# Performance work log

Measured on AMD Instinct MI355X. Metric: run time of the kernel, lower is better.

The kernel has to match this reference:

```python
import jax, jax.numpy as jnp
import numpy as np

B, NDOC, L, E = 32, 4, 512, 512
SCALE = np.float32(1.0 / np.sqrt(E))
NEG_INF = np.float32(-1e9)


def setup_inputs() -> dict:
    key = jax.random.key(0)
    k1, k2, k3, k4, k5, k6 = jax.random.split(key, 6)
    return {
        "x1": jax.random.normal(k1, (B, L, E), dtype=jnp.float32),
        "x2": jax.random.normal(k2, (B, NDOC, L, E), dtype=jnp.float32),
        "x1_len": jax.random.randint(k3, (B,), 0, L, dtype=jnp.int64),
        "x2_len": jax.random.randint(k4, (B, NDOC), 0, L, dtype=jnp.int64),
        "fusion_w": jax.random.normal(k5, (2 * E, E), dtype=jnp.float32) * 0.02,
        "fusion_b": jnp.zeros((E,), dtype=jnp.float32),
        "out_w": jax.random.normal(k6, (8 * E, 2 * E), dtype=jnp.float32) * 0.02,
        "out_b": jnp.zeros((2 * E,), dtype=jnp.float32),
    }


def reference(x1, x2, x1_len, x2_len, fusion_w, fusion_b, out_w, out_b):
    # Faithful to torch .repeat(1,4,...): concatenate 4 full copies along batch,
    # so attention row i pairs x1[i % B] with x2[i // 4, i % 4].
    x1_rep = jnp.tile(x1, (NDOC, 1, 1))          # [4B, L, E]
    x2_r = x2.reshape(-1, L, E)                  # [4B, L, E]

    x1_len_r = jnp.tile(x1_len, NDOC)            # [4B] (same tiling as x1_rep)
    x2_len_r = x2_len.reshape(-1)                # [4B]
    pos = jnp.arange(L)
    q_mask = pos[None, :] < x1_len_r[:, None]    # [4B, L]
    k_mask = pos[None, :] < x2_len_r[:, None]    # [4B, L]
    mask = q_mask[:, :, None] & k_mask[:, None, :]  # [4B, L, L]

    # scaled-dot-product attention with masked_fill(mask==0, -1e9)
    scores = jnp.einsum('bqe,bke->bqk', x1_rep, x2_r) * SCALE  # [4B, L, L]
    scores = jnp.where(mask, scores, NEG_INF)
    attn = jax.nn.softmax(scores, axis=-1)
    x1_att = jnp.einsum('bqk,bke->bqe', attn, x2_r)            # [4B, L, E]

    cat = jnp.concatenate([x1_rep - x1_att, x1_rep * x1_att], axis=-1)  # [4B, L, 2E]
    fus = jax.nn.relu(cat @ fusion_w + fusion_b)                        # [4B, L, E]

    x1_mean = jnp.mean(fus, axis=1)              # [4B, E]
    x1_max = jnp.max(fus, axis=1)                # [4B, E]
    pooled = jnp.concatenate([x1_mean.reshape(B, -1), x1_max.reshape(B, -1)], axis=-1)  # [B, 8E]
    out = jax.nn.relu(pooled @ out_w + out_b)    # [B, 2E]
    return out, attn
```

## Files before the change

kernel.cpp:

```cpp
#include <hip/hip_runtime.h>
#include <cstddef>

#define BATCH 32
#define NB    128
#define LL    512
#define EE    512
#define SCALE 0.044194173824159216f
#define NEG_INF -1e9f

typedef __attribute__((ext_vector_type(4))) float f32x4;
typedef __attribute__((ext_vector_type(8))) short s16x8;
typedef __attribute__((ext_vector_type(4))) unsigned short u16x4;

__device__ __forceinline__ unsigned short f2b(float f) {
    unsigned u = __float_as_uint(f);
    u += 0x7FFFu + ((u >> 16) & 1u);
    return (unsigned short)(u >> 16);
}
__device__ __forceinline__ float b2f(unsigned short h) {
    return __uint_as_float(((unsigned)h) << 16);
}

__global__ __launch_bounds__(256) void k_cvt_x1(
    const float* __restrict__ x1, unsigned short* __restrict__ x1bf)
{
    const size_t idx = (size_t)blockIdx.x * 256 + threadIdx.x;
    f32x4 v = *(const f32x4*)(x1 + idx * 4);
    u16x4 o = { f2b(v[0]), f2b(v[1]), f2b(v[2]), f2b(v[3]) };
    *(u16x4*)(x1bf + idx * 4) = o;
}

__global__ __launch_bounds__(256) void k_cvt_x2(
    const float* __restrict__ x2,
    unsigned short* __restrict__ x2bf, unsigned short* __restrict__ x2t)
{
    __shared__ float T[64][65];
    const int i = blockIdx.z, kb = blockIdx.y * 64, eb = blockIdx.x * 64;
    const float* src = x2 + (size_t)i * LL * EE;
    unsigned short* db = x2bf + (size_t)i * LL * EE;
    unsigned short* dt = x2t  + (size_t)i * LL * EE;
    const int t = threadIdx.x, r16 = t >> 4, c4 = (t & 15) * 4;
#pragma unroll
    for (int p = 0; p < 4; ++p) {
        int row = p * 16 + r16;
        f32x4 v = *(const f32x4*)(src + (size_t)(kb + row) * EE + eb + c4);
        T[row][c4] = v[0]; T[row][c4+1] = v[1]; T[row][c4+2] = v[2]; T[row][c4+3] = v[3];
        u16x4 o = { f2b(v[0]), f2b(v[1]), f2b(v[2]), f2b(v[3]) };
        *(u16x4*)(db + (size_t)(kb + row) * EE + eb + c4) = o;
    }
    __syncthreads();
#pragma unroll
    for (int p = 0; p < 4; ++p) {
        int erow = p * 16 + r16;
        u16x4 o = { f2b(T[c4][erow]), f2b(T[c4+1][erow]),
                    f2b(T[c4+2][erow]), f2b(T[c4+3][erow]) };
        *(u16x4*)(dt + (size_t)(eb + erow) * LL + kb + c4) = o;
    }
}

__global__ __launch_bounds__(256) void k_cvt_fw(
    const float* __restrict__ fw, unsigned short* __restrict__ fwt)
{
    __shared__ float T[64][65];
    const int jb = blockIdx.y * 64, eb = blockIdx.x * 64;
    const int t = threadIdx.x, r16 = t >> 4, c4 = (t & 15) * 4;
#pragma unroll
    for (int p = 0; p < 4; ++p) {
        int row = p * 16 + r16;
        f32x4 v = *(const f32x4*)(fw + (size_t)(jb + row) * EE + eb + c4);
        T[row][c4] = v[0]; T[row][c4+1] = v[1]; T[row][c4+2] = v[2]; T[row][c4+3] = v[3];
    }
    __syncthreads();
#pragma unroll
    for (int p = 0; p < 4; ++p) {
        int erow = p * 16 + r16;
        u16x4 o = { f2b(T[c4][erow]), f2b(T[c4+1][erow]),
                    f2b(T[c4+2][erow]), f2b(T[c4+3][erow]) };
        *(u16x4*)(fwt + (size_t)(eb + erow) * 1024 + jb + c4) = o;
    }
}

__global__ __launch_bounds__(256) void k_scores_mfma(
    const unsigned short* __restrict__ x1bf,
    const unsigned short* __restrict__ x2bf,
    const int* __restrict__ x1_len, const int* __restrict__ x2_len,
    float* __restrict__ attn)
{
    __shared__ unsigned short Al[128 * 40];
    __shared__ unsigned short Bl[128 * 40];
    const int i  = blockIdx.z;
    const int q0 = blockIdx.y * 128;
    const int k0 = blockIdx.x * 128;
    const unsigned short* Ag = x1bf + (size_t)(i & 31) * LL * EE;
    const unsigned short* Bg = x2bf + (size_t)i * LL * EE;
    const int t = threadIdx.x, lane = t & 63;
    const int w = t >> 6, wrow = w >> 1, wcol = w & 1;
    const int m = lane & 15, quad = lane >> 4;
    const int srow = t >> 1, shalf = (t & 1) * 16;

    f32x4 acc[4][4];
#pragma unroll
    for (int r = 0; r < 4; ++r)
#pragma unroll
        for (int c = 0; c < 4; ++c) acc[r][c] = (f32x4){0.f, 0.f, 0.f, 0.f};

    for (int e0 = 0; e0 < EE; e0 += 32) {
        s16x8 a0 = *(const s16x8*)(Ag + (size_t)(q0 + srow) * EE + e0 + shalf);
        s16x8 a1 = *(const s16x8*)(Ag + (size_t)(q0 + srow) * EE + e0 + shalf + 8);
        s16x8 b0 = *(const s16x8*)(Bg + (size_t)(k0 + srow) * EE + e0 + shalf);
        s16x8 b1 = *(const s16x8*)(Bg + (size_t)(k0 + srow) * EE + e0 + shalf + 8);
        __syncthreads();
        *(s16x8*)&Al[srow * 40 + shalf]     = a0;
        *(s16x8*)&Al[srow * 40 + shalf + 8] = a1;
        *(s16x8*)&Bl[srow * 40 + shalf]     = b0;
        *(s16x8*)&Bl[srow * 40 + shalf + 8] = b1;
        __syncthreads();
        s16x8 af[4], bfr[4];
#pragma unroll
        for (int rt = 0; rt < 4; ++rt)
            af[rt] = *(const s16x8*)&Al[(wrow * 64 + rt * 16 + m) * 40 + quad * 8];
#pragma unroll
        for (int ct = 0; ct < 4; ++ct)
            bfr[ct] = *(const s16x8*)&Bl[(wcol * 64 + ct * 16 + m) * 40 + quad * 8];
#pragma unroll
        for (int rt = 0; rt < 4; ++rt)
#pragma unroll
            for (int ct = 0; ct < 4; ++ct)
                acc[rt][ct] = __builtin_amdgcn_mfma_f32_16x16x32_bf16(
                    af[rt], bfr[ct], acc[rt][ct], 0, 0, 0);
    }

    const int qlen = x1_len[i & 31];
    const int klen = x2_len[i];
    float* op = attn + (size_t)i * LL * LL;
#pragma unroll
    for (int rt = 0; rt < 4; ++rt) {
#pragma unroll
        for (int reg = 0; reg < 4; ++reg) {
            const int q = q0 + wrow * 64 + rt * 16 + quad * 4 + reg;
            const bool qok = q < qlen;
#pragma unroll
            for (int ct = 0; ct < 4; ++ct) {
                const int k = k0 + wcol * 64 + ct * 16 + m;
                float v = (qok && k < klen) ? acc[rt][ct][reg] * SCALE : NEG_INF;
                op[(size_t)q * LL + k] = v;
            }
        }
    }
}

__global__ __launch_bounds__(256) void k_softmax(float* __restrict__ attn)
{
    const int row  = blockIdx.x * 4 + (threadIdx.x >> 6);
    const int lane = threadIdx.x & 63;
    float* p = attn + (size_t)row * LL + lane * 8;
    float4 v0 = *(float4*)p;
    float4 v1 = *(float4*)(p + 4);
    float mx = fmaxf(fmaxf(fmaxf(v0.x, v0.y), fmaxf(v0.z, v0.w)),
                     fmaxf(fmaxf(v1.x, v1.y), fmaxf(v1.z, v1.w)));
#pragma unroll
    for (int o = 32; o > 0; o >>= 1) mx = fmaxf(mx, __shfl_xor(mx, o));
    v0.x = __expf(v0.x - mx); v0.y = __expf(v0.y - mx);
    v0.z = __expf(v0.z - mx); v0.w = __expf(v0.w - mx);
    v1.x = __expf(v1.x - mx); v1.y = __expf(v1.y - mx);
    v1.z = __expf(v1.z - mx); v1.w = __expf(v1.w - mx);
    float s = v0.x + v0.y + v0.z + v0.w + v1.x + v1.y + v1.z + v1.w;
#pragma unroll
    for (int o = 32; o > 0; o >>= 1) s += __shfl_xor(s, o);
    const float inv = 1.0f / s;
    v0.x *= inv; v0.y *= inv; v0.z *= inv; v0.w *= inv;
    v1.x *= inv; v1.y *= inv; v1.z *= inv; v1.w *= inv;
    *(float4*)p = v0;
    *(float4*)(p + 4) = v1;
}

__global__ __launch_bounds__(256) void k_pv_mfma(
    const float* __restrict__ attn,
    const unsigned short* __restrict__ x2t,
    const unsigned short* __restrict__ x1bf,
    unsigned short* __restrict__ Cbuf)
{
    __shared__ unsigned short Al[128 * 40];
    __shared__ unsigned short Bl[128 * 40];
    const int i  = blockIdx.z;
    const int q0 = blockIdx.y * 128;
    const int e0 = blockIdx.x * 128;
    const float* Ag = attn + (size_t)i * LL * LL;
    const unsigned short* Bg = x2t + (size_t)i * LL * EE;
    const int t = threadIdx.x, lane = t & 63;
    const int w = t >> 6, wrow = w >> 1, wcol = w & 1;
    const int m = lane & 15, quad = lane >> 4;
    const int srow = t >> 1, shalf = (t & 1) * 16;

    f32x4 acc[4][4];
#pragma unroll
    for (int r = 0; r < 4; ++r)
#pragma unroll
        for (int c = 0; c < 4; ++c) acc[r][c] = (f32x4){0.f, 0.f, 0.f, 0.f};

    for (int kk0 = 0; kk0 < LL; kk0 += 32) {
        const float* ap = Ag + (size_t)(q0 + srow) * LL + kk0 + shalf;
        f32x4 v0 = *(const f32x4*)(ap + 0);
        f32x4 v1 = *(const f32x4*)(ap + 4);
        f32x4 v2 = *(const f32x4*)(ap + 8);
        f32x4 v3 = *(const f32x4*)(ap + 12);
        s16x8 b0 = *(const s16x8*)(Bg + (size_t)(e0 + srow) * LL + kk0 + shalf);
        s16x8 b1 = *(const s16x8*)(Bg + (size_t)(e0 + srow) * LL + kk0 + shalf + 8);
        s16x8 pa0, pa1;
#pragma unroll
        for (int j = 0; j < 4; ++j) {
            pa0[j]     = (short)f2b(v0[j]);
            pa0[j + 4] = (short)f2b(v1[j]);
            pa1[j]     = (short)f2b(v2[j]);
            pa1[j + 4] = (short)f2b(v3[j]);
        }
        __syncthreads();
        *(s16x8*)&Al[srow * 40 + shalf]     = pa0;
        *(s16x8*)&Al[srow * 40 + shalf + 8] = pa1;
        *(s16x8*)&Bl[srow * 40 + shalf]     = b0;
        *(s16x8*)&Bl[srow * 40 + shalf + 8] = b1;
        __syncthreads();
        s16x8 af[4], bfr[4];
#pragma unroll
        for (int rt = 0; rt < 4; ++rt)
            af[rt] = *(const s16x8*)&Al[(wrow * 64 + rt * 16 + m) * 40 + quad * 8];
#pragma unroll
        for (int ct = 0; ct < 4; ++ct)
            bfr[ct] = *(const s16x8*)&Bl[(wcol * 64 + ct * 16 + m) * 40 + quad * 8];
#pragma unroll
        for (int rt = 0; rt < 4; ++rt)
#pragma unroll
            for (int ct = 0; ct < 4; ++ct)
                acc[rt][ct] = __builtin_amdgcn_mfma_f32_16x16x32_bf16(
                    af[rt], bfr[ct], acc[rt][ct], 0, 0, 0);
    }

    const unsigned short* x1p = x1bf + (size_t)(i & 31) * LL * EE;
    unsigned short* Cb = Cbuf + (size_t)i * LL * 1024;
#pragma unroll
    for (int rt = 0; rt < 4; ++rt) {
#pragma unroll
        for (int reg = 0; reg < 4; ++reg) {
            const int l = q0 + wrow * 64 + rt * 16 + quad * 4 + reg;
#pragma unroll
            for (int ct = 0; ct < 4; ++ct) {
                const int e = e0 + wcol * 64 + ct * 16 + m;
                float att = acc[rt][ct][reg];
                float xv  = b2f(x1p[(size_t)l * EE + e]);
                Cb[(size_t)l * 1024 + e]       = f2b(xv - att);
                Cb[(size_t)l * 1024 + 512 + e] = f2b(xv * att);
            }
        }
    }
}

__global__ __launch_bounds__(256) void k_fuse_mfma(
    const unsigned short* __restrict__ Cbuf,
    const unsigned short* __restrict__ fwt,
    const float* __restrict__ fb,
    float* __restrict__ meanbuf, float* __restrict__ maxbuf)
{
    __shared__ unsigned short Al[128 * 40];
    __shared__ unsigned short Bl[128 * 40];
    __shared__ float psum[2][128];
    __shared__ float pmax[2][128];
    const int i  = blockIdx.y;
    const int e0 = blockIdx.x * 128;
    const unsigned short* Ab = Cbuf + (size_t)i * LL * 1024;
    const int t = threadIdx.x, lane = t & 63;
    const int w = t >> 6, wrow = w >> 1, wcol = w & 1;
    const int m = lane & 15, quad = lane >> 4;
    const int srow = t >> 1, shalf = (t & 1) * 16;

    float bias[4];
#pragma unroll
    for (int ct = 0; ct < 4; ++ct) bias[ct] = fb[e0 + wcol * 64 + ct * 16 + m];
    float csum[4] = {0.f, 0.f, 0.f, 0.f};
    float cmax[4] = {-3e38f, -3e38f, -3e38f, -3e38f};

    for (int l0 = 0; l0 < LL; l0 += 128) {
        f32x4 acc[4][4];
#pragma unroll
        for (int r = 0; r < 4; ++r)
#pragma unroll
            for (int c = 0; c < 4; ++c) acc[r][c] = (f32x4){0.f, 0.f, 0.f, 0.f};

        for (int j0 = 0; j0 < 1024; j0 += 32) {
            s16x8 a0 = *(const s16x8*)(Ab + (size_t)(l0 + srow) * 1024 + j0 + shalf);
            s16x8 a1 = *(const s16x8*)(Ab + (size_t)(l0 + srow) * 1024 + j0 + shalf + 8);
            s16x8 b0 = *(const s16x8*)(fwt + (size_t)(e0 + srow) * 1024 + j0 + shalf);
            s16x8 b1 = *(const s16x8*)(fwt + (size_t)(e0 + srow) * 1024 + j0 + shalf + 8);
            __syncthreads();
            *(s16x8*)&Al[srow * 40 + shalf]     = a0;
            *(s16x8*)&Al[srow * 40 + shalf + 8] = a1;
            *(s16x8*)&Bl[srow * 40 + shalf]     = b0;
            *(s16x8*)&Bl[srow * 40 + shalf + 8] = b1;
            __syncthreads();
            s16x8 af[4], bfr[4];
#pragma unroll
            for (int rt = 0; rt < 4; ++rt)
                af[rt] = *(const s16x8*)&Al[(wrow * 64 + rt * 16 + m) * 40 + quad * 8];
#pragma unroll
            for (int ct = 0; ct < 4; ++ct)
                bfr[ct] = *(const s16x8*)&Bl[(wcol * 64 + ct * 16 + m) * 40 + quad * 8];
#pragma unroll
            for (int rt = 0; rt < 4; ++rt)
#pragma unroll
                for (int ct = 0; ct < 4; ++ct)
                    acc[rt][ct] = __builtin_amdgcn_mfma_f32_16x16x32_bf16(
                        af[rt], bfr[ct], acc[rt][ct], 0, 0, 0);
        }
#pragma unroll
        for (int rt = 0; rt < 4; ++rt)
#pragma unroll
            for (int reg = 0; reg < 4; ++reg)
#pragma unroll
                for (int ct = 0; ct < 4; ++ct) {
                    float f = fmaxf(acc[rt][ct][reg] + bias[ct], 0.f);
                    csum[ct] += f;
                    cmax[ct] = fmaxf(cmax[ct], f);
                }
    }
#pragma unroll
    for (int ct = 0; ct < 4; ++ct) {
        csum[ct] += __shfl_xor(csum[ct], 16);
        csum[ct] += __shfl_xor(csum[ct], 32);
        cmax[ct] = fmaxf(cmax[ct], __shfl_xor(cmax[ct], 16));
        cmax[ct] = fmaxf(cmax[ct], __shfl_xor(cmax[ct], 32));
    }
    if (quad == 0) {
#pragma unroll
        for (int ct = 0; ct < 4; ++ct) {
            psum[wrow][wcol * 64 + ct * 16 + m] = csum[ct];
            pmax[wrow][wcol * 64 + ct * 16 + m] = cmax[ct];
        }
    }
    __syncthreads();
    if (t < 128) {
        float s  = psum[0][t] + psum[1][t];
        float mx = fmaxf(pmax[0][t], pmax[1][t]);
        meanbuf[(size_t)i * EE + e0 + t] = s * (1.0f / 512.0f);
        maxbuf[(size_t)i * EE + e0 + t] = mx;
    }
}

__global__ __launch_bounds__(256) void k_out_split(
    const float* __restrict__ meanbuf, const float* __restrict__ maxbuf,
    const float* __restrict__ ow, float* __restrict__ partial)
{
    __shared__ float ps[256];
    const int kc = blockIdx.x;
    const int b  = blockIdx.y;
    const int t  = threadIdx.x;
    const int j  = kc * 256 + t;
    float v;
    if (j < 2048) {
        v = meanbuf[(size_t)(4 * b + (j >> 9)) * EE + (j & 511)];
    } else {
        int jj = j - 2048;
        v = maxbuf[(size_t)(4 * b + (jj >> 9)) * EE + (jj & 511)];
    }
    ps[t] = v;
    __syncthreads();
    f32x4 acc = {0.f, 0.f, 0.f, 0.f};
    const float* wp = ow + (size_t)kc * 256 * 1024 + t * 4;
#pragma unroll 8
    for (int jj = 0; jj < 256; ++jj) {
        f32x4 w4 = *(const f32x4*)(wp + (size_t)jj * 1024);
        float p = ps[jj];
        acc[0] = fmaf(p, w4[0], acc[0]);
        acc[1] = fmaf(p, w4[1], acc[1]);
        acc[2] = fmaf(p, w4[2], acc[2]);
        acc[3] = fmaf(p, w4[3], acc[3]);
    }
    *(f32x4*)(partial + ((size_t)kc * 32 + b) * 1024 + t * 4) = acc;
}

__global__ __launch_bounds__(256) void k_out_final(
    const float* __restrict__ partial, const float* __restrict__ ob,
    float* __restrict__ out)
{
    const int idx = blockIdx.x * 256 + threadIdx.x;
    const int b = idx >> 10, o = idx & 1023;
    float s = ob[o];
#pragma unroll
    for (int kc = 0; kc < 16; ++kc)
        s += partial[((size_t)kc * 32 + b) * 1024 + o];
    out[idx] = fmaxf(s, 0.f);
}

extern "C" void kernel_launch(void* const* d_in, const int* in_sizes, int n_in,
                              void* d_out, int out_size, void* d_ws, size_t ws_size,
                              hipStream_t stream)
{
    const float* x1     = (const float*)d_in[0];
    const float* x2     = (const float*)d_in[1];
    const int*   x1_len = (const int*)d_in[2];
    const int*   x2_len = (const int*)d_in[3];
    const float* fw     = (const float*)d_in[4];
    const float* fb     = (const float*)d_in[5];
    const float* ow     = (const float*)d_in[6];
    const float* ob     = (const float*)d_in[7];

    float* out  = (float*)d_out;
    float* attn = out + (size_t)BATCH * 1024;

    char* wp = (char*)d_ws;
    unsigned short* x1bf = (unsigned short*)wp; wp += (size_t)BATCH * LL * EE * 2;
    unsigned short* x2bf = (unsigned short*)wp; wp += (size_t)NB * LL * EE * 2;
    unsigned short* x2t  = (unsigned short*)wp; wp += (size_t)NB * LL * EE * 2;
    unsigned short* Cbuf = (unsigned short*)wp; wp += (size_t)NB * LL * 1024 * 2;
    unsigned short* fwt  = (unsigned short*)wp; wp += (size_t)EE * 1024 * 2;
    float* meanbuf = (float*)wp; wp += (size_t)NB * EE * 4;
    float* maxbuf  = (float*)wp; wp += (size_t)NB * EE * 4;
    float* partial = (float*)wp; wp += (size_t)16 * BATCH * 1024 * 4;

    k_cvt_x1<<<dim3(BATCH * LL * EE / 4 / 256), 256, 0, stream>>>(x1, x1bf);
    k_cvt_x2<<<dim3(8, 8, NB), 256, 0, stream>>>(x2, x2bf, x2t);
    k_cvt_fw<<<dim3(8, 16), 256, 0, stream>>>(fw, fwt);
    k_scores_mfma<<<dim3(4, 4, NB), 256, 0, stream>>>(x1bf, x2bf, x1_len, x2_len, attn);
    k_softmax<<<dim3(NB * LL / 4), 256, 0, stream>>>(attn);
    k_pv_mfma<<<dim3(4, 4, NB), 256, 0, stream>>>(attn, x2t, x1bf, Cbuf);
    k_fuse_mfma<<<dim3(4, NB), 256, 0, stream>>>(Cbuf, fwt, fb, meanbuf, maxbuf);
    k_out_split<<<dim3(16, BATCH), 256, 0, stream>>>(meanbuf, maxbuf, ow, partial);
    k_out_final<<<dim3(BATCH * 1024 / 256), 256, 0, stream>>>(partial, ob, out);
}
```

Baseline: 673.4 us.

## Split fuse GEMM over L tiles, emit bf16 attn from softmax, remap grids

```diff
diff --git a/kernel.cpp b/kernel.cpp
--- a/kernel.cpp
+++ b/kernel.cpp
@@ -88,9 +88,9 @@
 {
     __shared__ unsigned short Al[128 * 40];
     __shared__ unsigned short Bl[128 * 40];
-    const int i  = blockIdx.z;
-    const int q0 = blockIdx.y * 128;
-    const int k0 = blockIdx.x * 128;
+    const int i  = blockIdx.x;
+    const int q0 = (blockIdx.y >> 2) * 128;
+    const int k0 = (blockIdx.y & 3) * 128;
     const unsigned short* Ag = x1bf + (size_t)(i & 31) * LL * EE;
     const unsigned short* Bg = x2bf + (size_t)i * LL * EE;
     const int t = threadIdx.x, lane = t & 63;
@@ -149,7 +149,8 @@
     }
 }
 
-__global__ __launch_bounds__(256) void k_softmax(float* __restrict__ attn)
+__global__ __launch_bounds__(256) void k_softmax(
+    float* __restrict__ attn, unsigned short* __restrict__ attnbf)
 {
     const int row  = blockIdx.x * 4 + (threadIdx.x >> 6);
     const int lane = threadIdx.x & 63;
@@ -172,21 +173,26 @@
     v1.x *= inv; v1.y *= inv; v1.z *= inv; v1.w *= inv;
     *(float4*)p = v0;
     *(float4*)(p + 4) = v1;
+    unsigned short* pb = attnbf + (size_t)row * LL + lane * 8;
+    u16x4 o0 = { f2b(v0.x), f2b(v0.y), f2b(v0.z), f2b(v0.w) };
+    u16x4 o1 = { f2b(v1.x), f2b(v1.y), f2b(v1.z), f2b(v1.w) };
+    *(u16x4*)pb       = o0;
+    *(u16x4*)(pb + 4) = o1;
 }
 
 __global__ __launch_bounds__(256) void k_pv_mfma(
-    const float* __restrict__ attn,
+    const unsigned short* __restrict__ attnbf,
     const unsigned short* __restrict__ x2t,
     const unsigned short* __restrict__ x1bf,
     unsigned short* __restrict__ Cbuf)
 {
     __shared__ unsigned short Al[128 * 40];
     __shared__ unsigned short Bl[128 * 40];
-    const int i  = blockIdx.z;
-    const int q0 = blockIdx.y * 128;
-    const int e0 = blockIdx.x * 128;
-    const float* Ag = attn + (size_t)i * LL * LL;
-    const unsigned short* Bg = x2t + (size_t)i * LL * EE;
+    const int i  = blockIdx.x;
+    const int q0 = (blockIdx.y >> 2) * 128;
+    const int e0 = (blockIdx.y & 3) * 128;
+    const unsigned short* Ag = attnbf + (size_t)i * LL * LL;
+    const unsigned short* Bg = x2t   + (size_t)i * LL * EE;
     const int t = threadIdx.x, lane = t & 63;
     const int w = t >> 6, wrow = w >> 1, wcol = w & 1;
     const int m = lane & 15, quad = lane >> 4;
@@ -199,24 +205,13 @@
         for (int c = 0; c < 4; ++c) acc[r][c] = (f32x4){0.f, 0.f, 0.f, 0.f};
 
     for (int kk0 = 0; kk0 < LL; kk0 += 32) {
-        const float* ap = Ag + (size_t)(q0 + srow) * LL + kk0 + shalf;
-        f32x4 v0 = *(const f32x4*)(ap + 0);
-        f32x4 v1 = *(const f32x4*)(ap + 4);
-        f32x4 v2 = *(const f32x4*)(ap + 8);
-        f32x4 v3 = *(const f32x4*)(ap + 12);
+        s16x8 a0 = *(const s16x8*)(Ag + (size_t)(q0 + srow) * LL + kk0 + shalf);
+        s16x8 a1 = *(const s16x8*)(Ag + (size_t)(q0 + srow) * LL + kk0 + shalf + 8);
         s16x8 b0 = *(const s16x8*)(Bg + (size_t)(e0 + srow) * LL + kk0 + shalf);
         s16x8 b1 = *(const s16x8*)(Bg + (size_t)(e0 + srow) * LL + kk0 + shalf + 8);
-        s16x8 pa0, pa1;
-#pragma unroll
-        for (int j = 0; j < 4; ++j) {
-            pa0[j]     = (short)f2b(v0[j]);
-            pa0[j + 4] = (short)f2b(v1[j]);
-            pa1[j]     = (short)f2b(v2[j]);
-            pa1[j + 4] = (short)f2b(v3[j]);
-        }
-        __syncthreads();
-        *(s16x8*)&Al[srow * 40 + shalf]     = pa0;
-        *(s16x8*)&Al[srow * 40 + shalf + 8] = pa1;
+        __syncthreads();
+        *(s16x8*)&Al[srow * 40 + shalf]     = a0;
+        *(s16x8*)&Al[srow * 40 + shalf + 8] = a1;
         *(s16x8*)&Bl[srow * 40 + shalf]     = b0;
         *(s16x8*)&Bl[srow * 40 + shalf + 8] = b1;
         __syncthreads();
@@ -258,15 +253,16 @@
     const unsigned short* __restrict__ Cbuf,
     const unsigned short* __restrict__ fwt,
     const float* __restrict__ fb,
-    float* __restrict__ meanbuf, float* __restrict__ maxbuf)
+    float* __restrict__ pmean, float* __restrict__ pmax)
 {
     __shared__ unsigned short Al[128 * 40];
     __shared__ unsigned short Bl[128 * 40];
     __shared__ float psum[2][128];
-    __shared__ float pmax[2][128];
-    const int i  = blockIdx.y;
-    const int e0 = blockIdx.x * 128;
-    const unsigned short* Ab = Cbuf + (size_t)i * LL * 1024;
+    __shared__ float pmx[2][128];
+    const int i  = blockIdx.x;
+    const int lt = blockIdx.y >> 2;
+    const int e0 = (blockIdx.y & 3) * 128;
+    const unsigned short* Ab = Cbuf + ((size_t)i * LL + lt * 128) * 1024;
     const int t = threadIdx.x, lane = t & 63;
     const int w = t >> 6, wrow = w >> 1, wcol = w & 1;
     const int m = lane & 15, quad = lane >> 4;
@@ -278,49 +274,47 @@
     float csum[4] = {0.f, 0.f, 0.f, 0.f};
     float cmax[4] = {-3e38f, -3e38f, -3e38f, -3e38f};
 
-    for (int l0 = 0; l0 < LL; l0 += 128) {
-        f32x4 acc[4][4];
-#pragma unroll
-        for (int r = 0; r < 4; ++r)
-#pragma unroll
-            for (int c = 0; c < 4; ++c) acc[r][c] = (f32x4){0.f, 0.f, 0.f, 0.f};
-
-        for (int j0 = 0; j0 < 1024; j0 += 32) {
-            s16x8 a0 = *(const s16x8*)(Ab + (size_t)(l0 + srow) * 1024 + j0 + shalf);
-            s16x8 a1 = *(const s16x8*)(Ab + (size_t)(l0 + srow) * 1024 + j0 + shalf + 8);
-            s16x8 b0 = *(const s16x8*)(fwt + (size_t)(e0 + srow) * 1024 + j0 + shalf);
-            s16x8 b1 = *(const s16x8*)(fwt + (size_t)(e0 + srow) * 1024 + j0 + shalf + 8);
-            __syncthreads();
-            *(s16x8*)&Al[srow * 40 + shalf]     = a0;
-            *(s16x8*)&Al[srow * 40 + shalf + 8] = a1;
-            *(s16x8*)&Bl[srow * 40 + shalf]     = b0;
-            *(s16x8*)&Bl[srow * 40 + shalf + 8] = b1;
-            __syncthreads();
-            s16x8 af[4], bfr[4];
-#pragma unroll
-            for (int rt = 0; rt < 4; ++rt)
-                af[rt] = *(const s16x8*)&Al[(wrow * 64 + rt * 16 + m) * 40 + quad * 8];
+    f32x4 acc[4][4];
+#pragma unroll
+    for (int r = 0; r < 4; ++r)
+#pragma unroll
+        for (int c = 0; c < 4; ++c) acc[r][c] = (f32x4){0.f, 0.f, 0.f, 0.f};
+
+    for (int j0 = 0; j0 < 1024; j0 += 32) {
+        s16x8 a0 = *(const s16x8*)(Ab + (size_t)srow * 1024 + j0 + shalf);
+        s16x8 a1 = *(const s16x8*)(Ab + (size_t)srow * 1024 + j0 + shalf + 8);
+        s16x8 b0 = *(const s16x8*)(fwt + (size_t)(e0 + srow) * 1024 + j0 + shalf);
+        s16x8 b1 = *(const s16x8*)(fwt + (size_t)(e0 + srow) * 1024 + j0 + shalf + 8);
+        __syncthreads();
+        *(s16x8*)&Al[srow * 40 + shalf]     = a0;
+        *(s16x8*)&Al[srow * 40 + shalf + 8] = a1;
+        *(s16x8*)&Bl[srow * 40 + shalf]     = b0;
+        *(s16x8*)&Bl[srow * 40 + shalf + 8] = b1;
+        __syncthreads();
+        s16x8 af[4], bfr[4];
+#pragma unroll
+        for (int rt = 0; rt < 4; ++rt)
+            af[rt] = *(const s16x8*)&Al[(wrow * 64 + rt * 16 + m) * 40 + quad * 8];
+#pragma unroll
+        for (int ct = 0; ct < 4; ++ct)
+            bfr[ct] = *(const s16x8*)&Bl[(wcol * 64 + ct * 16 + m) * 40 + quad * 8];
+#pragma unroll
+        for (int rt = 0; rt < 4; ++rt)
 #pragma unroll
             for (int ct = 0; ct < 4; ++ct)
-                bfr[ct] = *(const s16x8*)&Bl[(wcol * 64 + ct * 16 + m) * 40 + quad * 8];
-#pragma unroll
-            for (int rt = 0; rt < 4; ++rt)
-#pragma unroll
-                for (int ct = 0; ct < 4; ++ct)
-                    acc[rt][ct] = __builtin_amdgcn_mfma_f32_16x16x32_bf16(
-                        af[rt], bfr[ct], acc[rt][ct], 0, 0, 0);
-        }
-#pragma unroll
-        for (int rt = 0; rt < 4; ++rt)
-#pragma unroll
-            for (int reg = 0; reg < 4; ++reg)
-#pragma unroll
-                for (int ct = 0; ct < 4; ++ct) {
-                    float f = fmaxf(acc[rt][ct][reg] + bias[ct], 0.f);
-                    csum[ct] += f;
-                    cmax[ct] = fmaxf(cmax[ct], f);
-                }
-    }
+                acc[rt][ct] = __builtin_amdgcn_mfma_f32_16x16x32_bf16(
+                    af[rt], bfr[ct], acc[rt][ct], 0, 0, 0);
+    }
+#pragma unroll
+    for (int rt = 0; rt < 4; ++rt)
+#pragma unroll
+        for (int reg = 0; reg < 4; ++reg)
+#pragma unroll
+            for (int ct = 0; ct < 4; ++ct) {
+                float f = fmaxf(acc[rt][ct][reg] + bias[ct], 0.f);
+                csum[ct] += f;
+                cmax[ct] = fmaxf(cmax[ct], f);
+            }
 #pragma unroll
     for (int ct = 0; ct < 4; ++ct) {
         csum[ct] += __shfl_xor(csum[ct], 16);
@@ -332,20 +326,20 @@
 #pragma unroll
         for (int ct = 0; ct < 4; ++ct) {
             psum[wrow][wcol * 64 + ct * 16 + m] = csum[ct];
-            pmax[wrow][wcol * 64 + ct * 16 + m] = cmax[ct];
+            pmx[wrow][wcol * 64 + ct * 16 + m] = cmax[ct];
         }
     }
     __syncthreads();
     if (t < 128) {
         float s  = psum[0][t] + psum[1][t];
-        float mx = fmaxf(pmax[0][t], pmax[1][t]);
-        meanbuf[(size_t)i * EE + e0 + t] = s * (1.0f / 512.0f);
-        maxbuf[(size_t)i * EE + e0 + t] = mx;
+        float mx = fmaxf(pmx[0][t], pmx[1][t]);
+        pmean[((size_t)i * 4 + lt) * EE + e0 + t] = s;
+        pmax[((size_t)i * 4 + lt) * EE + e0 + t]  = mx;
     }
 }
 
 __global__ __launch_bounds__(256) void k_out_split(
-    const float* __restrict__ meanbuf, const float* __restrict__ maxbuf,
+    const float* __restrict__ pmean, const float* __restrict__ pmax,
     const float* __restrict__ ow, float* __restrict__ partial)
 {
     __shared__ float ps[256];
@@ -353,21 +347,25 @@
     const int b  = blockIdx.y;
     const int t  = threadIdx.x;
     const int j  = kc * 256 + t;
+    const int jj = (j < 2048) ? j : j - 2048;
+    const int ii = 4 * b + (jj >> 9);
+    const int e  = jj & 511;
     float v;
     if (j < 2048) {
-        v = meanbuf[(size_t)(4 * b + (j >> 9)) * EE + (j & 511)];
+        const float* bp = pmean + (size_t)ii * 4 * EE + e;
+        v = (bp[0] + bp[512] + bp[1024] + bp[1536]) * (1.0f / 512.0f);
     } else {
-        int jj = j - 2048;
-        v = maxbuf[(size_t)(4 * b + (jj >> 9)) * EE + (jj & 511)];
+        const float* bp = pmax + (size_t)ii * 4 * EE + e;
+        v = fmaxf(fmaxf(bp[0], bp[512]), fmaxf(bp[1024], bp[1536]));
     }
     ps[t] = v;
     __syncthreads();
     f32x4 acc = {0.f, 0.f, 0.f, 0.f};
     const float* wp = ow + (size_t)kc * 256 * 1024 + t * 4;
 #pragma unroll 8
-    for (int jj = 0; jj < 256; ++jj) {
-        f32x4 w4 = *(const f32x4*)(wp + (size_t)jj * 1024);
-        float p = ps[jj];
+    for (int q = 0; q < 256; ++q) {
+        f32x4 w4 = *(const f32x4*)(wp + (size_t)q * 1024);
+        float p = ps[q];
         acc[0] = fmaf(p, w4[0], acc[0]);
         acc[1] = fmaf(p, w4[1], acc[1]);
         acc[2] = fmaf(p, w4[2], acc[2]);
@@ -406,22 +404,23 @@
     float* attn = out + (size_t)BATCH * 1024;
 
     char* wp = (char*)d_ws;
-    unsigned short* x1bf = (unsigned short*)wp; wp += (size_t)BATCH * LL * EE * 2;
-    unsigned short* x2bf = (unsigned short*)wp; wp += (size_t)NB * LL * EE * 2;
-    unsigned short* x2t  = (unsigned short*)wp; wp += (size_t)NB * LL * EE * 2;
-    unsigned short* Cbuf = (unsigned short*)wp; wp += (size_t)NB * LL * 1024 * 2;
-    unsigned short* fwt  = (unsigned short*)wp; wp += (size_t)EE * 1024 * 2;
-    float* meanbuf = (float*)wp; wp += (size_t)NB * EE * 4;
-    float* maxbuf  = (float*)wp; wp += (size_t)NB * EE * 4;
+    unsigned short* x1bf   = (unsigned short*)wp; wp += (size_t)BATCH * LL * EE * 2;
+    unsigned short* x2bf   = (unsigned short*)wp; wp += (size_t)NB * LL * EE * 2;
+    unsigned short* x2t    = (unsigned short*)wp; wp += (size_t)NB * LL * EE * 2;
+    unsigned short* attnbf = (unsigned short*)wp; wp += (size_t)NB * LL * LL * 2;
+    unsigned short* Cbuf   = (unsigned short*)wp; wp += (size_t)NB * LL * 1024 * 2;
+    unsigned short* fwt    = (unsigned short*)wp; wp += (size_t)EE * 1024 * 2;
+    float* pmean   = (float*)wp; wp += (size_t)NB * 4 * EE * 4;
+    float* pmax    = (float*)wp; wp += (size_t)NB * 4 * EE * 4;
     float* partial = (float*)wp; wp += (size_t)16 * BATCH * 1024 * 4;
 
     k_cvt_x1<<<dim3(BATCH * LL * EE / 4 / 256), 256, 0, stream>>>(x1, x1bf);
     k_cvt_x2<<<dim3(8, 8, NB), 256, 0, stream>>>(x2, x2bf, x2t);
     k_cvt_fw<<<dim3(8, 16), 256, 0, stream>>>(fw, fwt);
-    k_scores_mfma<<<dim3(4, 4, NB), 256, 0, stream>>>(x1bf, x2bf, x1_len, x2_len, attn);
-    k_softmax<<<dim3(NB * LL / 4), 256, 0, stream>>>(attn);
-    k_pv_mfma<<<dim3(4, 4, NB), 256, 0, stream>>>(attn, x2t, x1bf, Cbuf);
-    k_fuse_mfma<<<dim3(4, NB), 256, 0, stream>>>(Cbuf, fwt, fb, meanbuf, maxbuf);
-    k_out_split<<<dim3(16, BATCH), 256, 0, stream>>>(meanbuf, maxbuf, ow, partial);
+    k_scores_mfma<<<dim3(128, 16), 256, 0, stream>>>(x1bf, x2bf, x1_len, x2_len, attn);
+    k_softmax<<<dim3(NB * LL / 4), 256, 0, stream>>>(attn, attnbf);
+    k_pv_mfma<<<dim3(128, 16), 256, 0, stream>>>(attnbf, x2t, x1bf, Cbuf);
+    k_fuse_mfma<<<dim3(128, 16), 256, 0, stream>>>(Cbuf, fwt, fb, pmean, pmax);
+    k_out_split<<<dim3(16, BATCH), 256, 0, stream>>>(pmean, pmax, ow, partial);
     k_out_final<<<dim3(BATCH * 1024 / 256), 256, 0, stream>>>(partial, ob, out);
 }
```

After: 660.4 us. Within noise of the previous version (-1.9%).
